# Kernel optimization log

Measured on AMD Instinct MI355X. Metric: run time of the kernel, lower is better.

Reference implementation:

```python
import jax, jax.numpy as jnp
import numpy as np


def _binarize_ste(w):
    # forward: sign(w) in {-1, +1}; backward: identity (straight-through)
    wb = jnp.where(w >= 0, 1.0, -1.0).astype(w.dtype)
    return w + jax.lax.stop_gradient(wb - w)


def setup_inputs() -> dict:
    key = jax.random.key(0)
    k1, k2 = jax.random.split(key)
    IN, OUT, N = 2048, 2048, 8192
    x = jax.random.normal(k1, (N, IN), dtype=jnp.float32)
    # kaiming_uniform-like init: U(-bound, bound), bound = sqrt(6/in)*? (gain sqrt(5) default in torch)
    bound = float(np.sqrt(6.0 / IN))
    weight = jax.random.uniform(k2, (OUT, IN), dtype=jnp.float32, minval=-bound, maxval=bound)
    bias = jnp.zeros((OUT,), dtype=jnp.float32)
    return {"x": x, "weight": weight, "bias": bias}


def reference(x, weight, bias):
    w_binary = _binarize_ste(weight)  # [out, in], values in {-1, +1}
    # F.linear: x @ W^T + b
    return jnp.einsum('ni,oi->no', x, w_binary) + bias
```

## Files before the change

kernel.cpp:

```cpp
#include <hip/hip_runtime.h>
#include <hip/hip_bf16.h>
#include <stdint.h>


typedef __bf16 bf16x8 __attribute__((ext_vector_type(8)));
typedef float f32x4 __attribute__((ext_vector_type(4)));

typedef const __attribute__((address_space(1))) void* gas_ptr;
typedef __attribute__((address_space(3))) void* lds_ptr;

__device__ __forceinline__ unsigned short f2bf_rne(float f) {
    unsigned int u = __builtin_bit_cast(unsigned int, f);
    u += 0x7fffu + ((u >> 16) & 1u);
    return (unsigned short)(u >> 16);
}

__global__ __launch_bounds__(256) void cvt_x_kernel(const float* __restrict__ in,
                                                    unsigned short* __restrict__ out,
                                                    int n8) {
    int i = blockIdx.x * 256 + threadIdx.x;
    if (i >= n8) return;
    const float4* p = reinterpret_cast<const float4*>(in + (size_t)i * 8);
    float4 f0 = p[0], f1 = p[1];
    union { unsigned short s[8]; uint4 v; } o;
    o.s[0] = f2bf_rne(f0.x); o.s[1] = f2bf_rne(f0.y);
    o.s[2] = f2bf_rne(f0.z); o.s[3] = f2bf_rne(f0.w);
    o.s[4] = f2bf_rne(f1.x); o.s[5] = f2bf_rne(f1.y);
    o.s[6] = f2bf_rne(f1.z); o.s[7] = f2bf_rne(f1.w);
    *reinterpret_cast<uint4*>(out + (size_t)i * 8) = o.v;
}

__global__ __launch_bounds__(256) void bin_w_kernel(const float* __restrict__ in,
                                                    unsigned short* __restrict__ out,
                                                    int n8) {
    int i = blockIdx.x * 256 + threadIdx.x;
    if (i >= n8) return;
    const float4* p = reinterpret_cast<const float4*>(in + (size_t)i * 8);
    float4 f0 = p[0], f1 = p[1];
    union { unsigned short s[8]; uint4 v; } o;
    o.s[0] = (f0.x >= 0.f) ? 0x3F80u : 0xBF80u;
    o.s[1] = (f0.y >= 0.f) ? 0x3F80u : 0xBF80u;
    o.s[2] = (f0.z >= 0.f) ? 0x3F80u : 0xBF80u;
    o.s[3] = (f0.w >= 0.f) ? 0x3F80u : 0xBF80u;
    o.s[4] = (f1.x >= 0.f) ? 0x3F80u : 0xBF80u;
    o.s[5] = (f1.y >= 0.f) ? 0x3F80u : 0xBF80u;
    o.s[6] = (f1.z >= 0.f) ? 0x3F80u : 0xBF80u;
    o.s[7] = (f1.w >= 0.f) ? 0x3F80u : 0xBF80u;
    *reinterpret_cast<uint4*>(out + (size_t)i * 8) = o.v;
}

#define TILE 128
#define BK   32

__global__ __launch_bounds__(256) void gemm_bin_kernel(
    const unsigned short* __restrict__ A,
    const unsigned short* __restrict__ B,
    const float* __restrict__ bias,
    float* __restrict__ C,
    int M, int N, int K)
{
    __shared__ unsigned short Als[TILE * BK];
    __shared__ unsigned short Bls[TILE * BK];

    const int tid  = threadIdx.x;
    const int lane = tid & 63;
    const int wave = tid >> 6;
    const int wm   = wave & 1;
    const int wn   = wave >> 1;

    const int bm = blockIdx.y;
    const int bn = blockIdx.x;

    const unsigned short* Ag = A + (size_t)bm * TILE * K;
    const unsigned short* Bg = B + (size_t)bn * TILE * K;

    const int g0 = tid;
    const int g1 = 256 + tid;
    const int r0 = g0 >> 2, c0 = (g0 & 3) * 8;
    const int r1 = g1 >> 2, c1 = (g1 & 3) * 8;

    f32x4 acc[4][4];
#pragma unroll
    for (int a = 0; a < 4; ++a)
#pragma unroll
        for (int b = 0; b < 4; ++b)
            acc[a][b] = {0.f, 0.f, 0.f, 0.f};

    const int laneM = lane & 15;
    const int laneQ = lane >> 4;
    const int ldsKOff = laneQ * 8;

    for (int k0 = 0; k0 < K; k0 += BK) {
        __builtin_amdgcn_global_load_lds(
            (gas_ptr)(Ag + (size_t)r0 * K + k0 + c0),
            (lds_ptr)(&Als[g0 * 8]), 16, 0, 0);
        __builtin_amdgcn_global_load_lds(
            (gas_ptr)(Ag + (size_t)r1 * K + k0 + c1),
            (lds_ptr)(&Als[g1 * 8]), 16, 0, 0);
        __builtin_amdgcn_global_load_lds(
            (gas_ptr)(Bg + (size_t)r0 * K + k0 + c0),
            (lds_ptr)(&Bls[g0 * 8]), 16, 0, 0);
        __builtin_amdgcn_global_load_lds(
            (gas_ptr)(Bg + (size_t)r1 * K + k0 + c1),
            (lds_ptr)(&Bls[g1 * 8]), 16, 0, 0);

        __syncthreads();

        bf16x8 af[4], bfr[4];
#pragma unroll
        for (int mi = 0; mi < 4; ++mi) {
            int row = wm * 64 + mi * 16 + laneM;
            af[mi] = *reinterpret_cast<const bf16x8*>(&Als[row * BK + ldsKOff]);
        }
#pragma unroll
        for (int ni = 0; ni < 4; ++ni) {
            int row = wn * 64 + ni * 16 + laneM;
            bfr[ni] = *reinterpret_cast<const bf16x8*>(&Bls[row * BK + ldsKOff]);
        }

#pragma unroll
        for (int mi = 0; mi < 4; ++mi)
#pragma unroll
            for (int ni = 0; ni < 4; ++ni)
                acc[mi][ni] = __builtin_amdgcn_mfma_f32_16x16x32_bf16(
                    af[mi], bfr[ni], acc[mi][ni], 0, 0, 0);

        __syncthreads();
    }

    const int colBase = bn * TILE + wn * 64 + laneM;
    const int rowBase = bm * TILE + wm * 64 + laneQ * 4;
#pragma unroll
    for (int ni = 0; ni < 4; ++ni) {
        int col = colBase + ni * 16;
        float bv = bias[col];
#pragma unroll
        for (int mi = 0; mi < 4; ++mi) {
            int row = rowBase + mi * 16;
#pragma unroll
            for (int r = 0; r < 4; ++r) {
                C[(size_t)(row + r) * N + col] = acc[mi][ni][r] + bv;
            }
        }
    }
}

extern "C" void kernel_launch(void* const* d_in, const int* in_sizes, int n_in,
                              void* d_out, int out_size, void* d_ws, size_t ws_size,
                              hipStream_t stream) {
    const float* x    = (const float*)d_in[0];
    const float* w    = (const float*)d_in[1];
    const float* bias = (const float*)d_in[2];
    float* out = (float*)d_out;

    const int K = 2048;
    const int N = in_sizes[2];
    const int M = in_sizes[0] / K;

    unsigned short* xb = (unsigned short*)d_ws;
    unsigned short* wb = xb + (size_t)M * K;

    const int nx8 = (M * K) / 8;
    const int nw8 = (N * K) / 8;
    cvt_x_kernel<<<(nx8 + 255) / 256, 256, 0, stream>>>(x, xb, nx8);
    bin_w_kernel<<<(nw8 + 255) / 256, 256, 0, stream>>>(w, wb, nw8);

    dim3 grid(N / TILE, M / TILE);
    gemm_bin_kernel<<<grid, 256, 0, stream>>>(xb, wb, bias, out, M, N, K);
}
```

Before: 232.2 us.

## Fuse fp32-to-bf16 activation conversion into GEMM and coalesce epilogue via LDS

Removes the separate activation conversion kernel; the GEMM now loads fp32 X into registers with one-step prefetch, converts to bf16 and writes to LDS while binarized weights still use direct global-to-LDS loads. The epilogue stages accumulators through LDS so each thread writes float4 rows with bias added, replacing scattered scalar stores. This avoids a round trip of the bf16 activation buffer, but each column block now reads fp32 activations, doubling A-side read bytes and adding conversion ALU inside the main loop.

```diff
diff --git a/kernel.cpp b/kernel.cpp
--- a/kernel.cpp
+++ b/kernel.cpp
@@ -1,5 +1,4 @@
 #include <hip/hip_runtime.h>
-#include <hip/hip_bf16.h>
 #include <stdint.h>
 
 
@@ -15,69 +14,59 @@
     return (unsigned short)(u >> 16);
 }
 
-__global__ __launch_bounds__(256) void cvt_x_kernel(const float* __restrict__ in,
-                                                    unsigned short* __restrict__ out,
-                                                    int n8) {
-    int i = blockIdx.x * 256 + threadIdx.x;
-    if (i >= n8) return;
-    const float4* p = reinterpret_cast<const float4*>(in + (size_t)i * 8);
-    float4 f0 = p[0], f1 = p[1];
+__device__ __forceinline__ uint4 pack8(float4 a, float4 b) {
     union { unsigned short s[8]; uint4 v; } o;
-    o.s[0] = f2bf_rne(f0.x); o.s[1] = f2bf_rne(f0.y);
-    o.s[2] = f2bf_rne(f0.z); o.s[3] = f2bf_rne(f0.w);
-    o.s[4] = f2bf_rne(f1.x); o.s[5] = f2bf_rne(f1.y);
-    o.s[6] = f2bf_rne(f1.z); o.s[7] = f2bf_rne(f1.w);
-    *reinterpret_cast<uint4*>(out + (size_t)i * 8) = o.v;
+    o.s[0] = f2bf_rne(a.x); o.s[1] = f2bf_rne(a.y);
+    o.s[2] = f2bf_rne(a.z); o.s[3] = f2bf_rne(a.w);
+    o.s[4] = f2bf_rne(b.x); o.s[5] = f2bf_rne(b.y);
+    o.s[6] = f2bf_rne(b.z); o.s[7] = f2bf_rne(b.w);
+    return o.v;
 }
 
 __global__ __launch_bounds__(256) void bin_w_kernel(const float* __restrict__ in,
                                                     unsigned short* __restrict__ out,
-                                                    int n8) {
+                                                    int n4) {
     int i = blockIdx.x * 256 + threadIdx.x;
-    if (i >= n8) return;
-    const float4* p = reinterpret_cast<const float4*>(in + (size_t)i * 8);
-    float4 f0 = p[0], f1 = p[1];
-    union { unsigned short s[8]; uint4 v; } o;
-    o.s[0] = (f0.x >= 0.f) ? 0x3F80u : 0xBF80u;
-    o.s[1] = (f0.y >= 0.f) ? 0x3F80u : 0xBF80u;
-    o.s[2] = (f0.z >= 0.f) ? 0x3F80u : 0xBF80u;
-    o.s[3] = (f0.w >= 0.f) ? 0x3F80u : 0xBF80u;
-    o.s[4] = (f1.x >= 0.f) ? 0x3F80u : 0xBF80u;
-    o.s[5] = (f1.y >= 0.f) ? 0x3F80u : 0xBF80u;
-    o.s[6] = (f1.z >= 0.f) ? 0x3F80u : 0xBF80u;
-    o.s[7] = (f1.w >= 0.f) ? 0x3F80u : 0xBF80u;
-    *reinterpret_cast<uint4*>(out + (size_t)i * 8) = o.v;
+    if (i >= n4) return;
+    float4 f = reinterpret_cast<const float4*>(in)[i];
+    union { unsigned short s[4]; uint2 v; } o;
+    o.s[0] = (f.x >= 0.f) ? 0x3F80u : 0xBF80u;
+    o.s[1] = (f.y >= 0.f) ? 0x3F80u : 0xBF80u;
+    o.s[2] = (f.z >= 0.f) ? 0x3F80u : 0xBF80u;
+    o.s[3] = (f.w >= 0.f) ? 0x3F80u : 0xBF80u;
+    reinterpret_cast<uint2*>(out)[i] = o.v;
 }
 
 #define TILE 128
 #define BK   32
 
-__global__ __launch_bounds__(256) void gemm_bin_kernel(
-    const unsigned short* __restrict__ A,
-    const unsigned short* __restrict__ B,
+__global__ __launch_bounds__(256) void gemm_fused_kernel(
+    const float* __restrict__ X,
+    const unsigned short* __restrict__ Bw,
     const float* __restrict__ bias,
     float* __restrict__ C,
     int M, int N, int K)
 {
-    __shared__ unsigned short Als[TILE * BK];
-    __shared__ unsigned short Bls[TILE * BK];
+    __shared__ __align__(16) unsigned char smem[16384];
+    unsigned short* Als = (unsigned short*)smem;
+    unsigned short* Bls = (unsigned short*)(smem + 8192);
 
     const int tid  = threadIdx.x;
     const int lane = tid & 63;
     const int wave = tid >> 6;
     const int wm   = wave & 1;
     const int wn   = wave >> 1;
+    const int bm   = blockIdx.y;
+    const int bn   = blockIdx.x;
 
-    const int bm = blockIdx.y;
-    const int bn = blockIdx.x;
+    const int r0 = tid >> 2;
+    const int r1 = r0 + 64;
+    const int kc = (tid & 3) * 8;
 
-    const unsigned short* Ag = A + (size_t)bm * TILE * K;
-    const unsigned short* Bg = B + (size_t)bn * TILE * K;
-
-    const int g0 = tid;
-    const int g1 = 256 + tid;
-    const int r0 = g0 >> 2, c0 = (g0 & 3) * 8;
-    const int r1 = g1 >> 2, c1 = (g1 & 3) * 8;
+    const float*          Ag0 = X  + (size_t)(bm * TILE + r0) * K + kc;
+    const float*          Ag1 = Ag0 + (size_t)64 * K;
+    const unsigned short* Bg0 = Bw + (size_t)(bn * TILE + r0) * K + kc;
+    const unsigned short* Bg1 = Bg0 + (size_t)64 * K;
 
     f32x4 acc[4][4];
 #pragma unroll
@@ -88,21 +77,30 @@
 
     const int laneM = lane & 15;
     const int laneQ = lane >> 4;
-    const int ldsKOff = laneQ * 8;
+    const int koff  = laneQ * 8;
+
+    float4 pa0 = *(const float4*)(Ag0);
+    float4 pa1 = *(const float4*)(Ag0 + 4);
+    float4 pb0 = *(const float4*)(Ag1);
+    float4 pb1 = *(const float4*)(Ag1 + 4);
 
     for (int k0 = 0; k0 < K; k0 += BK) {
-        __builtin_amdgcn_global_load_lds(
-            (gas_ptr)(Ag + (size_t)r0 * K + k0 + c0),
-            (lds_ptr)(&Als[g0 * 8]), 16, 0, 0);
-        __builtin_amdgcn_global_load_lds(
-            (gas_ptr)(Ag + (size_t)r1 * K + k0 + c1),
-            (lds_ptr)(&Als[g1 * 8]), 16, 0, 0);
-        __builtin_amdgcn_global_load_lds(
-            (gas_ptr)(Bg + (size_t)r0 * K + k0 + c0),
-            (lds_ptr)(&Bls[g0 * 8]), 16, 0, 0);
-        __builtin_amdgcn_global_load_lds(
-            (gas_ptr)(Bg + (size_t)r1 * K + k0 + c1),
-            (lds_ptr)(&Bls[g1 * 8]), 16, 0, 0);
+        __syncthreads();
+
+        __builtin_amdgcn_global_load_lds((gas_ptr)(Bg0 + k0),
+                                         (lds_ptr)&Bls[r0 * BK + kc], 16, 0, 0);
+        __builtin_amdgcn_global_load_lds((gas_ptr)(Bg1 + k0),
+                                         (lds_ptr)&Bls[r1 * BK + kc], 16, 0, 0);
+
+        *reinterpret_cast<uint4*>(&Als[r0 * BK + kc]) = pack8(pa0, pa1);
+        *reinterpret_cast<uint4*>(&Als[r1 * BK + kc]) = pack8(pb0, pb1);
+
+        if (k0 + BK < K) {
+            pa0 = *(const float4*)(Ag0 + k0 + BK);
+            pa1 = *(const float4*)(Ag0 + k0 + BK + 4);
+            pb0 = *(const float4*)(Ag1 + k0 + BK);
+            pb1 = *(const float4*)(Ag1 + k0 + BK + 4);
+        }
 
         __syncthreads();
 
@@ -110,12 +108,12 @@
 #pragma unroll
         for (int mi = 0; mi < 4; ++mi) {
             int row = wm * 64 + mi * 16 + laneM;
-            af[mi] = *reinterpret_cast<const bf16x8*>(&Als[row * BK + ldsKOff]);
+            af[mi] = *reinterpret_cast<const bf16x8*>(&Als[row * BK + koff]);
         }
 #pragma unroll
         for (int ni = 0; ni < 4; ++ni) {
             int row = wn * 64 + ni * 16 + laneM;
-            bfr[ni] = *reinterpret_cast<const bf16x8*>(&Bls[row * BK + ldsKOff]);
+            bfr[ni] = *reinterpret_cast<const bf16x8*>(&Bls[row * BK + koff]);
         }
 
 #pragma unroll
@@ -124,23 +122,28 @@
             for (int ni = 0; ni < 4; ++ni)
                 acc[mi][ni] = __builtin_amdgcn_mfma_f32_16x16x32_bf16(
                     af[mi], bfr[ni], acc[mi][ni], 0, 0, 0);
-
-        __syncthreads();
     }
 
-    const int colBase = bn * TILE + wn * 64 + laneM;
-    const int rowBase = bm * TILE + wm * 64 + laneQ * 4;
+    float* eps = (float*)smem + wave * 1024;
+    const int ec = laneM * 4;
+    float4 bv = *(const float4*)&bias[bn * TILE + wn * 64 + ec];
+
 #pragma unroll
-    for (int ni = 0; ni < 4; ++ni) {
-        int col = colBase + ni * 16;
-        float bv = bias[col];
+    for (int mi = 0; mi < 4; ++mi) {
+        __syncthreads();
 #pragma unroll
-        for (int mi = 0; mi < 4; ++mi) {
-            int row = rowBase + mi * 16;
+        for (int ni = 0; ni < 4; ++ni)
 #pragma unroll
-            for (int r = 0; r < 4; ++r) {
-                C[(size_t)(row + r) * N + col] = acc[mi][ni][r] + bv;
-            }
+            for (int r = 0; r < 4; ++r)
+                eps[(laneQ * 4 + r) * 64 + ni * 16 + laneM] = acc[mi][ni][r];
+        __syncthreads();
+#pragma unroll
+        for (int kk = 0; kk < 4; ++kk) {
+            int rl = kk * 4 + laneQ;
+            float4 v = *reinterpret_cast<const float4*>(&eps[rl * 64 + ec]);
+            float4 o = {v.x + bv.x, v.y + bv.y, v.z + bv.z, v.w + bv.w};
+            size_t grow = (size_t)(bm * TILE + wm * 64 + mi * 16 + rl);
+            *reinterpret_cast<float4*>(&C[grow * N + bn * TILE + wn * 64 + ec]) = o;
         }
     }
 }
@@ -157,14 +160,11 @@
     const int N = in_sizes[2];
     const int M = in_sizes[0] / K;
 
-    unsigned short* xb = (unsigned short*)d_ws;
-    unsigned short* wb = xb + (size_t)M * K;
+    unsigned short* wb = (unsigned short*)d_ws;
 
-    const int nx8 = (M * K) / 8;
-    const int nw8 = (N * K) / 8;
-    cvt_x_kernel<<<(nx8 + 255) / 256, 256, 0, stream>>>(x, xb, nx8);
-    bin_w_kernel<<<(nw8 + 255) / 256, 256, 0, stream>>>(w, wb, nw8);
+    const int nw4 = (N * K) / 4;
+    bin_w_kernel<<<(nw4 + 255) / 256, 256, 0, stream>>>(w, wb, nw4);
 
     dim3 grid(N / TILE, M / TILE);
-    gemm_bin_kernel<<<grid, 256, 0, stream>>>(xb, wb, bias, out, M, N, K);
+    gemm_fused_kernel<<<grid, 256, 0, stream>>>(x, wb, bias, out, M, N, K);
 }
```

Result: faster. 223.6 us (-3.7%).

## Use 32x32x16 MFMA, BK=64 with XOR-swizzled LDS, and LDS-staged vectorized epilogue

Applied to the files above, without the earlier changes.

The GEMM moves from 16x16x32 to 32x32x16 bf16 MFMA tiles and doubles the K step to 64. LDS rows are XOR-swizzled so the fragment reads avoid bank conflicts. The epilogue stages accumulators through LDS so the output can be written as coalesced float4 stores with the bias added. The weight binarization kernel now uses a narrower per-thread vector width. Together these aim to cut LDS bank conflicts, reduce loop and sync overhead per MFMA, and fix the strided scalar output stores, at the cost of extra LDS traffic and barriers in the epilogue.

```diff
diff --git a/kernel.cpp b/kernel.cpp
--- a/kernel.cpp
+++ b/kernel.cpp
@@ -1,10 +1,9 @@
 #include <hip/hip_runtime.h>
-#include <hip/hip_bf16.h>
 #include <stdint.h>
 
 
 typedef __bf16 bf16x8 __attribute__((ext_vector_type(8)));
-typedef float f32x4 __attribute__((ext_vector_type(4)));
+typedef float f32x16 __attribute__((ext_vector_type(16)));
 
 typedef const __attribute__((address_space(1))) void* gas_ptr;
 typedef __attribute__((address_space(3))) void* lds_ptr;
@@ -32,25 +31,20 @@
 
 __global__ __launch_bounds__(256) void bin_w_kernel(const float* __restrict__ in,
                                                     unsigned short* __restrict__ out,
-                                                    int n8) {
+                                                    int n4) {
     int i = blockIdx.x * 256 + threadIdx.x;
-    if (i >= n8) return;
-    const float4* p = reinterpret_cast<const float4*>(in + (size_t)i * 8);
-    float4 f0 = p[0], f1 = p[1];
-    union { unsigned short s[8]; uint4 v; } o;
-    o.s[0] = (f0.x >= 0.f) ? 0x3F80u : 0xBF80u;
-    o.s[1] = (f0.y >= 0.f) ? 0x3F80u : 0xBF80u;
-    o.s[2] = (f0.z >= 0.f) ? 0x3F80u : 0xBF80u;
-    o.s[3] = (f0.w >= 0.f) ? 0x3F80u : 0xBF80u;
-    o.s[4] = (f1.x >= 0.f) ? 0x3F80u : 0xBF80u;
-    o.s[5] = (f1.y >= 0.f) ? 0x3F80u : 0xBF80u;
-    o.s[6] = (f1.z >= 0.f) ? 0x3F80u : 0xBF80u;
-    o.s[7] = (f1.w >= 0.f) ? 0x3F80u : 0xBF80u;
-    *reinterpret_cast<uint4*>(out + (size_t)i * 8) = o.v;
+    if (i >= n4) return;
+    float4 f = reinterpret_cast<const float4*>(in)[i];
+    union { unsigned short s[4]; uint2 v; } o;
+    o.s[0] = (f.x >= 0.f) ? 0x3F80u : 0xBF80u;
+    o.s[1] = (f.y >= 0.f) ? 0x3F80u : 0xBF80u;
+    o.s[2] = (f.z >= 0.f) ? 0x3F80u : 0xBF80u;
+    o.s[3] = (f.w >= 0.f) ? 0x3F80u : 0xBF80u;
+    reinterpret_cast<uint2*>(out)[i] = o.v;
 }
 
 #define TILE 128
-#define BK   32
+#define BK   64
 
 __global__ __launch_bounds__(256) void gemm_bin_kernel(
     const unsigned short* __restrict__ A,
@@ -59,88 +53,110 @@
     float* __restrict__ C,
     int M, int N, int K)
 {
-    __shared__ unsigned short Als[TILE * BK];
-    __shared__ unsigned short Bls[TILE * BK];
+    __shared__ __align__(16) unsigned char smem[32768];
+    unsigned short* Als = (unsigned short*)smem;
+    unsigned short* Bls = (unsigned short*)(smem + 16384);
 
     const int tid  = threadIdx.x;
     const int lane = tid & 63;
     const int wave = tid >> 6;
     const int wm   = wave & 1;
     const int wn   = wave >> 1;
+    const int bm   = blockIdx.y;
+    const int bn   = blockIdx.x;
 
-    const int bm = blockIdx.y;
-    const int bn = blockIdx.x;
+    const unsigned short* Agb = A + (size_t)(bm * TILE) * K;
+    const unsigned short* Bgb = B + (size_t)(bn * TILE) * K;
 
-    const unsigned short* Ag = A + (size_t)bm * TILE * K;
-    const unsigned short* Bg = B + (size_t)bn * TILE * K;
+    f32x16 acc[2][2];
+#pragma unroll
+    for (int a = 0; a < 2; ++a)
+#pragma unroll
+        for (int b = 0; b < 2; ++b)
+#pragma unroll
+            for (int r = 0; r < 16; ++r)
+                acc[a][b][r] = 0.f;
 
-    const int g0 = tid;
-    const int g1 = 256 + tid;
-    const int r0 = g0 >> 2, c0 = (g0 & 3) * 8;
-    const int r1 = g1 >> 2, c1 = (g1 & 3) * 8;
+    const int lr  = lane & 31;
+    const int lk  = lane >> 5;
+    const int swz = lane & 7;
 
-    f32x4 acc[4][4];
+    int st_row[4], st_col[4];
 #pragma unroll
-    for (int a = 0; a < 4; ++a)
-#pragma unroll
-        for (int b = 0; b < 4; ++b)
-            acc[a][b] = {0.f, 0.f, 0.f, 0.f};
-
-    const int laneM = lane & 15;
-    const int laneQ = lane >> 4;
-    const int ldsKOff = laneQ * 8;
+    for (int j = 0; j < 4; ++j) {
+        int g = j * 256 + tid;
+        st_row[j] = g >> 3;
+        st_col[j] = ((g & 7) ^ (st_row[j] & 7)) * 8;
+    }
 
     for (int k0 = 0; k0 < K; k0 += BK) {
-        __builtin_amdgcn_global_load_lds(
-            (gas_ptr)(Ag + (size_t)r0 * K + k0 + c0),
-            (lds_ptr)(&Als[g0 * 8]), 16, 0, 0);
-        __builtin_amdgcn_global_load_lds(
-            (gas_ptr)(Ag + (size_t)r1 * K + k0 + c1),
-            (lds_ptr)(&Als[g1 * 8]), 16, 0, 0);
-        __builtin_amdgcn_global_load_lds(
-            (gas_ptr)(Bg + (size_t)r0 * K + k0 + c0),
-            (lds_ptr)(&Bls[g0 * 8]), 16, 0, 0);
-        __builtin_amdgcn_global_load_lds(
-            (gas_ptr)(Bg + (size_t)r1 * K + k0 + c1),
-            (lds_ptr)(&Bls[g1 * 8]), 16, 0, 0);
+        __syncthreads();
+
+#pragma unroll
+        for (int j = 0; j < 4; ++j) {
+            int g = j * 256 + tid;
+            __builtin_amdgcn_global_load_lds(
+                (gas_ptr)(Agb + (size_t)st_row[j] * K + k0 + st_col[j]),
+                (lds_ptr)&Als[g * 8], 16, 0, 0);
+        }
+#pragma unroll
+        for (int j = 0; j < 4; ++j) {
+            int g = j * 256 + tid;
+            __builtin_amdgcn_global_load_lds(
+                (gas_ptr)(Bgb + (size_t)st_row[j] * K + k0 + st_col[j]),
+                (lds_ptr)&Bls[g * 8], 16, 0, 0);
+        }
 
         __syncthreads();
 
-        bf16x8 af[4], bfr[4];
 #pragma unroll
-        for (int mi = 0; mi < 4; ++mi) {
-            int row = wm * 64 + mi * 16 + laneM;
-            af[mi] = *reinterpret_cast<const bf16x8*>(&Als[row * BK + ldsKOff]);
+        for (int ks = 0; ks < 4; ++ks) {
+            const int c = ks * 2 + lk;
+            bf16x8 af[2], bfv[2];
+#pragma unroll
+            for (int mi = 0; mi < 2; ++mi) {
+                int row = wm * 64 + mi * 32 + lr;
+                af[mi] = *reinterpret_cast<const bf16x8*>(
+                    &Als[(row * 8 + (c ^ swz)) * 8]);
+            }
+#pragma unroll
+            for (int ni = 0; ni < 2; ++ni) {
+                int row = wn * 64 + ni * 32 + lr;
+                bfv[ni] = *reinterpret_cast<const bf16x8*>(
+                    &Bls[(row * 8 + (c ^ swz)) * 8]);
+            }
+#pragma unroll
+            for (int mi = 0; mi < 2; ++mi)
+#pragma unroll
+                for (int ni = 0; ni < 2; ++ni)
+                    acc[mi][ni] = __builtin_amdgcn_mfma_f32_32x32x16_bf16(
+                        af[mi], bfv[ni], acc[mi][ni], 0, 0, 0);
         }
-#pragma unroll
-        for (int ni = 0; ni < 4; ++ni) {
-            int row = wn * 64 + ni * 16 + laneM;
-            bfr[ni] = *reinterpret_cast<const bf16x8*>(&Bls[row * BK + ldsKOff]);
-        }
+    }
+
+    float* eps = (float*)smem + wave * 2048;
+    const int c4 = (lane & 15) * 4;
+    const int pr = lane >> 4;
+    float4 bv = *(const float4*)&bias[bn * TILE + wn * 64 + c4];
 
 #pragma unroll
-        for (int mi = 0; mi < 4; ++mi)
+    for (int mi = 0; mi < 2; ++mi) {
+        __syncthreads();
 #pragma unroll
-            for (int ni = 0; ni < 4; ++ni)
-                acc[mi][ni] = __builtin_amdgcn_mfma_f32_16x16x32_bf16(
-                    af[mi], bfr[ni], acc[mi][ni], 0, 0, 0);
-
+        for (int ni = 0; ni < 2; ++ni)
+#pragma unroll
+            for (int r = 0; r < 16; ++r) {
+                int rl = (r & 3) + 8 * (r >> 2) + 4 * lk;
+                eps[rl * 64 + ni * 32 + lr] = acc[mi][ni][r];
+            }
         __syncthreads();
-    }
-
-    const int colBase = bn * TILE + wn * 64 + laneM;
-    const int rowBase = bm * TILE + wm * 64 + laneQ * 4;
 #pragma unroll
-    for (int ni = 0; ni < 4; ++ni) {
-        int col = colBase + ni * 16;
-        float bv = bias[col];
-#pragma unroll
-        for (int mi = 0; mi < 4; ++mi) {
-            int row = rowBase + mi * 16;
-#pragma unroll
-            for (int r = 0; r < 4; ++r) {
-                C[(size_t)(row + r) * N + col] = acc[mi][ni][r] + bv;
-            }
+        for (int p = 0; p < 8; ++p) {
+            int rl = p * 4 + pr;
+            float4 v = *reinterpret_cast<const float4*>(&eps[rl * 64 + c4]);
+            float4 o = {v.x + bv.x, v.y + bv.y, v.z + bv.z, v.w + bv.w};
+            size_t grow = (size_t)(bm * TILE + wm * 64 + mi * 32 + rl);
+            *reinterpret_cast<float4*>(&C[grow * N + bn * TILE + wn * 64 + c4]) = o;
         }
     }
 }
@@ -161,9 +177,9 @@
     unsigned short* wb = xb + (size_t)M * K;
 
     const int nx8 = (M * K) / 8;
-    const int nw8 = (N * K) / 8;
+    const int nw4 = (N * K) / 4;
     cvt_x_kernel<<<(nx8 + 255) / 256, 256, 0, stream>>>(x, xb, nx8);
-    bin_w_kernel<<<(nw8 + 255) / 256, 256, 0, stream>>>(w, wb, nw8);
+    bin_w_kernel<<<(nw4 + 255) / 256, 256, 0, stream>>>(w, wb, nw4);
 
     dim3 grid(N / TILE, M / TILE);
     gemm_bin_kernel<<<grid, 256, 0, stream>>>(xb, wb, bias, out, M, N, K);
```

Measured after the change: 200.8 us. 1.16x faster.
